# Kernel optimization log

Hardware: AMD Instinct MI355X
Metric: run time of the kernel (lower is better)

## Reference

```python
import jax, jax.numpy as jnp
import numpy as np
import math

V, T, E, H, L = 32000, 1024, 1024, 16, 6
B = 2
D = E // H
F = 4 * E


def setup_inputs() -> dict:
    key = jax.random.key(0)
    ks = jax.random.split(key, 12)
    s = 0.02
    rn = lambda k, shape: jax.random.normal(k, shape, jnp.float32) * s
    return dict(
        idx=jax.random.randint(ks[0], (B, T), 0, V),
        tok_w=rn(ks[1], (V, E)),
        pos_w=rn(ks[2], (T, E)),
        ln1_g=jnp.ones((L, E)), ln1_b=jnp.zeros((L, E)),
        wq=rn(ks[3], (L, E, E)), wk=rn(ks[4], (L, E, E)), wv=rn(ks[5], (L, E, E)),
        wp=rn(ks[6], (L, E, E)), bp=jnp.zeros((L, E)),
        ln2_g=jnp.ones((L, E)), ln2_b=jnp.zeros((L, E)),
        w1=rn(ks[7], (L, E, F)), b1=jnp.zeros((L, F)),
        w2=rn(ks[8], (L, F, E)), b2=jnp.zeros((L, E)),
        lnf_g=jnp.ones((E,)), lnf_b=jnp.zeros((E,)),
        wlm=rn(ks[9], (E, V)), blm=jnp.zeros((V,)),
    )


def _layernorm(x, g, b, eps=1e-5):
    m = jnp.mean(x, axis=-1, keepdims=True)
    v = jnp.var(x, axis=-1, keepdims=True)
    return (x - m) * jax.lax.rsqrt(v + eps) * g + b


def _forward(idx, tok_w, pos_w, ln1_g, ln1_b, wq, wk, wv, wp, bp,
             ln2_g, ln2_b, w1, b1, w2, b2, lnf_g, lnf_b, wlm, blm):
    Bx, Tx = idx.shape
    x = tok_w[idx] + pos_w[jnp.arange(Tx)][None, :, :]  # [B,T,E]
    causal = jnp.tril(jnp.ones((Tx, Tx), dtype=bool))
    scale = 1.0 / math.sqrt(D)
    for l in range(L):
        h = _layernorm(x, ln1_g[l], ln1_b[l])
        q = (h @ wq[l]).reshape(Bx, Tx, H, D).transpose(0, 2, 1, 3)  # [B,H,T,D]
        k = (h @ wk[l]).reshape(Bx, Tx, H, D).transpose(0, 2, 1, 3)
        v = (h @ wv[l]).reshape(Bx, Tx, H, D).transpose(0, 2, 1, 3)
        att = jnp.einsum('bhtd,bhsd->bhts', q, k) * scale  # [B,H,T,T]
        att = jnp.where(causal, att, -jnp.inf)
        att = jax.nn.softmax(att, axis=-1)
        y = jnp.einsum('bhts,bhsd->bhtd', att, v)
        y = y.transpose(0, 2, 1, 3).reshape(Bx, Tx, E)
        x = x + y @ wp[l] + bp[l]
        h2 = _layernorm(x, ln2_g[l], ln2_b[l])
        ff = jax.nn.gelu(h2 @ w1[l] + b1[l], approximate=False) @ w2[l] + b2[l]
        x = x + ff
    x = _layernorm(x, lnf_g, lnf_b)
    return x @ wlm + blm  # logits [B,T,V]


def reference(idx, tok_w, pos_w, ln1_g, ln1_b, wq, wk, wv, wp, bp,
              ln2_g, ln2_b, w1, b1, w2, b2, lnf_g, lnf_b, wlm, blm):
    return _forward(idx, tok_w, pos_w, ln1_g, ln1_b, wq, wk, wv, wp, bp,
                    ln2_g, ln2_b, w1, b1, w2, b2, lnf_g, lnf_b, wlm, blm)
```

## Files before the change

### kernel.cpp

```cpp
#include <hip/hip_runtime.h>

#define T_SEQ   1024
#define E_DIM   1024
#define H_HEADS 16
#define D_HEAD  64
#define L_LAYERS 6
#define B_BATCH 2
#define F_DIM   4096
#define V_VOCAB 32000

typedef float f32x4 __attribute__((ext_vector_type(4)));
typedef short short8 __attribute__((ext_vector_type(8)));

__device__ __forceinline__ unsigned short f2bf(float f) {
  union { float f; unsigned int u; } v; v.f = f;
  unsigned int r = v.u + 0x7fffu + ((v.u >> 16) & 1u);
  return (unsigned short)(r >> 16);
}

#define GLDS16(gp, lp) __builtin_amdgcn_global_load_lds( \
    (const __attribute__((address_space(1))) void*)(gp), \
    (__attribute__((address_space(3))) void*)(lp), 16, 0, 0)

__global__ void embed_kernel(const int* __restrict__ idx, const float* __restrict__ tok,
                             const float* __restrict__ pos, float* __restrict__ x) {
  int i = blockIdx.x * 256 + threadIdx.x;
  int bt = i >> 8;
  int e4 = i & 255;
  int t  = bt & (T_SEQ - 1);
  int tokid = idx[bt];
  f32x4 a = *(const f32x4*)(tok + (size_t)tokid * E_DIM + e4 * 4);
  f32x4 p = *(const f32x4*)(pos + (size_t)t * E_DIM + e4 * 4);
  *(f32x4*)(x + (size_t)bt * E_DIM + e4 * 4) = a + p;
}

__global__ void ln_kernel(const float* __restrict__ x, const float* __restrict__ g,
                          const float* __restrict__ b, unsigned short* __restrict__ out) {
  int row = blockIdx.x;
  int tid = threadIdx.x;
  const float* xr = x + (size_t)row * E_DIM;
  f32x4 v = *(const f32x4*)(xr + tid * 4);
  float s  = v[0] + v[1] + v[2] + v[3];
  float s2 = v[0]*v[0] + v[1]*v[1] + v[2]*v[2] + v[3]*v[3];
  #pragma unroll
  for (int off = 32; off > 0; off >>= 1) {
    s  += __shfl_xor(s,  off);
    s2 += __shfl_xor(s2, off);
  }
  __shared__ float red[2][4];
  int wave = tid >> 6;
  if ((tid & 63) == 0) { red[0][wave] = s; red[1][wave] = s2; }
  __syncthreads();
  s  = red[0][0] + red[0][1] + red[0][2] + red[0][3];
  s2 = red[1][0] + red[1][1] + red[1][2] + red[1][3];
  float mean = s * (1.0f / E_DIM);
  float var  = s2 * (1.0f / E_DIM) - mean * mean;
  float rstd = rsqrtf(var + 1e-5f);
  f32x4 gv = *(const f32x4*)(g + tid * 4);
  f32x4 bv = *(const f32x4*)(b + tid * 4);
  ushort4 o;
  o.x = f2bf((v[0] - mean) * rstd * gv[0] + bv[0]);
  o.y = f2bf((v[1] - mean) * rstd * gv[1] + bv[1]);
  o.z = f2bf((v[2] - mean) * rstd * gv[2] + bv[2]);
  o.w = f2bf((v[3] - mean) * rstd * gv[3] + bv[3]);
  *(ushort4*)(out + (size_t)row * E_DIM + tid * 4) = o;
}

__device__ __forceinline__ void wtrans_body(const float* __restrict__ W,
    unsigned short* __restrict__ Wt, int K, int N, int bx, int by) {
  __shared__ float tile[64][65];
  const int n0 = bx * 64, k0 = by * 64;
  const int tr  = threadIdx.x >> 4;
  const int tc4 = (threadIdx.x & 15) * 4;
  #pragma unroll
  for (int p = 0; p < 4; ++p) {
    f32x4 v = *(const f32x4*)(W + (size_t)(k0 + p * 16 + tr) * N + n0 + tc4);
    tile[p * 16 + tr][tc4 + 0] = v[0];
    tile[p * 16 + tr][tc4 + 1] = v[1];
    tile[p * 16 + tr][tc4 + 2] = v[2];
    tile[p * 16 + tr][tc4 + 3] = v[3];
  }
  __syncthreads();
  #pragma unroll
  for (int p = 0; p < 4; ++p) {
    int n = p * 16 + tr;
    ushort4 o;
    o.x = f2bf(tile[tc4 + 0][n]);
    o.y = f2bf(tile[tc4 + 1][n]);
    o.z = f2bf(tile[tc4 + 2][n]);
    o.w = f2bf(tile[tc4 + 3][n]);
    *(ushort4*)(Wt + (size_t)(n0 + n) * K + k0 + tc4) = o;
  }
}

__global__ __launch_bounds__(256) void wtrans_kernel(const float* __restrict__ W,
    unsigned short* __restrict__ Wt, int K, int N) {
  wtrans_body(W, Wt, K, N, blockIdx.x, blockIdx.y);
}

__global__ __launch_bounds__(256) void wtrans4_kernel(const float* __restrict__ W0,
    const float* __restrict__ W1, const float* __restrict__ W2, const float* __restrict__ W3,
    unsigned short* __restrict__ Wt) {
  const float* W = blockIdx.z == 0 ? W0 : (blockIdx.z == 1 ? W1 : (blockIdx.z == 2 ? W2 : W3));
  wtrans_body(W, Wt + (size_t)blockIdx.z * E_DIM * E_DIM, E_DIM, E_DIM,
              blockIdx.x, blockIdx.y);
}

__global__ __launch_bounds__(256) void wtrans2_kernel(const float* __restrict__ W1,
    const float* __restrict__ W2, unsigned short* __restrict__ Wt1,
    unsigned short* __restrict__ Wt2) {
  const int id = blockIdx.x;
  if (blockIdx.y == 0) wtrans_body(W1, Wt1, E_DIM, F_DIM, id % (F_DIM / 64), id / (F_DIM / 64));
  else                 wtrans_body(W2, Wt2, F_DIM, E_DIM, id % (E_DIM / 64), id / (E_DIM / 64));
}

__global__ __launch_bounds__(512) void attn_mfma_kernel(
    const unsigned short* __restrict__ qk, const unsigned short* __restrict__ vt,
    unsigned short* __restrict__ y) {
  __shared__ __align__(16) char smem[2 * 16384 + 8 * 1280 + 512];
  const int tid  = threadIdx.x;
  const int lane = tid & 63;
  const int wave = tid >> 6;
  const int wl = wave & 3;
  const int g  = wave >> 2;
  const int qx = blockIdx.x;
  const int h  = blockIdx.y & (H_HEADS - 1);
  const int b  = blockIdx.y >> 4;
  const int qt = b ? (15 - qx) : qx;
  const int r0 = qt * 64 + wl * 16;
  const size_t RS = 2 * E_DIM;
  const unsigned short* q  = qk + (size_t)b * T_SEQ * RS + (size_t)h * D_HEAD;
  const unsigned short* k  = q + E_DIM;
  const unsigned short* vb = vt + (size_t)(b * H_HEADS + h) * D_HEAD * T_SEQ;
  const size_t ybase = (size_t)b * T_SEQ * E_DIM + (size_t)h * D_HEAD;
  const int fr = lane & 15, fg = lane >> 4;
  const int srow = lane >> 3;
  const int ssw  = ((lane & 7) * 16) ^ (srow << 4);
  char* pb = smem + 32768 + wave * 1280;
  float* mlb = (float*)(smem + 32768 + 10240);

  short8 aq[2];
  #pragma unroll
  for (int c = 0; c < 2; ++c)
    aq[c] = *(const short8*)(q + (size_t)(r0 + fr) * RS + c * 32 + fg * 8);

  f32x4 oacc[4];
  #pragma unroll
  for (int cg = 0; cg < 4; ++cg) oacc[cg] = (f32x4){0.f, 0.f, 0.f, 0.f};
  float m_ = -1e30f, l_ = 0.0f;

  auto stage = [&](int t) {
    const int j0 = t * 64;
    char* Kd = smem + (t & 1) * 16384;
    GLDS16((const char*)k  + (size_t)(j0 + wave * 8 + srow) * RS * 2 + ssw,
           Kd + wave * 1024);
    GLDS16((const char*)vb + ((size_t)(wave * 8 + srow) * T_SEQ + j0) * 2 + ssw,
           Kd + 8192 + wave * 1024);
  };

  stage(0);
  for (int t = 0; t <= qt; ++t) {
    __builtin_amdgcn_sched_barrier(0);
    __builtin_amdgcn_s_barrier();
    if (t < qt) stage(t + 1);
    __builtin_amdgcn_sched_barrier(0);
    if (t < qt) asm volatile("s_waitcnt vmcnt(2)" ::: "memory");
    else        asm volatile("s_waitcnt vmcnt(0)" ::: "memory");
    __builtin_amdgcn_sched_barrier(0);
    __builtin_amdgcn_s_barrier();
    __builtin_amdgcn_sched_barrier(0);
    const char* Kl = smem + (t & 1) * 16384;
    const char* Vl = Kl + 8192;
    const int j0 = t * 64;
    if (!(t == qt && g == 1 && wl < 2)) {
      f32x4 st[2];
      #pragma unroll
      for (int cc = 0; cc < 2; ++cc) {
        const int kloc = g * 32 + cc * 16 + fr;
        const char* kb = Kl + kloc * 128;
        const int sw = (kloc & 7) << 4;
        short8 ka0 = *(const short8*)(kb + ((fg * 16) ^ sw));
        short8 ka1 = *(const short8*)(kb + ((64 + fg * 16) ^ sw));
        f32x4 z = (f32x4){0.f, 0.f, 0.f, 0.f};
        z = __builtin_amdgcn_mfma_f32_16x16x32_bf16(ka0, aq[0], z, 0, 0, 0);
        z = __builtin_amdgcn_mfma_f32_16x16x32_bf16(ka1, aq[1], z, 0, 0, 0);
        st[cc] = z;
      }
      const int qg = r0 + fr;
      float pv[2][4];
      float mx = -1e30f;
      #pragma unroll
      for (int cc = 0; cc < 2; ++cc)
        #pragma unroll
        for (int r = 0; r < 4; ++r) {
          const int kj = j0 + g * 32 + cc * 16 + fg * 4 + r;
          float val = (kj <= qg) ? st[cc][r] * 0.125f : -1e30f;
          pv[cc][r] = val;
          mx = fmaxf(mx, val);
        }
      mx = fmaxf(mx, __shfl_xor(mx, 16));
      mx = fmaxf(mx, __shfl_xor(mx, 32));
      const float mn = fmaxf(m_, mx);
      const float cfs = __expf(m_ - mn);
      float ls = 0.0f;
      #pragma unroll
      for (int cc = 0; cc < 2; ++cc) {
        ushort4 o;
        float e0 = pv[cc][0] > -1e29f ? __expf(pv[cc][0] - mn) : 0.0f;
        float e1 = pv[cc][1] > -1e29f ? __expf(pv[cc][1] - mn) : 0.0f;
        float e2 = pv[cc][2] > -1e29f ? __expf(pv[cc][2] - mn) : 0.0f;
        float e3 = pv[cc][3] > -1e29f ? __expf(pv[cc][3] - mn) : 0.0f;
        ls += (e0 + e1) + (e2 + e3);
        o.x = f2bf(e0); o.y = f2bf(e1); o.z = f2bf(e2); o.w = f2bf(e3);
        *(ushort4*)(pb + fr * 80 + cc * 32 + fg * 8) = o;
      }
      ls += __shfl_xor(ls, 16);
      ls += __shfl_xor(ls, 32);
      l_ = l_ * cfs + ls;
      m_ = mn;
      float cfO[4];
      #pragma unroll
      for (int r = 0; r < 4; ++r) cfO[r] = __shfl(cfs, (lane & 48) | (fg * 4 + r));
      asm volatile("s_waitcnt lgkmcnt(0)" ::: "memory");
      __builtin_amdgcn_sched_barrier(0);
      short8 pa = *(const short8*)(pb + fr * 80 + fg * 16);
      __builtin_amdgcn_s_setprio(1);
      #pragma unroll
      for (int cg = 0; cg < 4; ++cg) {
        const int d = cg * 16 + fr;
        short8 bv = *(const short8*)(Vl + d * 128 + ((g * 64 + fg * 16) ^ ((d & 7) << 4)));
        #pragma unroll
        for (int r = 0; r < 4; ++r) oacc[cg][r] *= cfO[r];
        oacc[cg] = __builtin_amdgcn_mfma_f32_16x16x32_bf16(pa, bv, oacc[cg], 0, 0, 0);
      }
      __builtin_amdgcn_s_setprio(0);
    }
  }
  __syncthreads();
  float* obuf = (float*)smem;
  if (g == 1) {
    #pragma unroll
    for (int cg = 0; cg < 4; ++cg)
      #pragma unroll
      for (int r = 0; r < 4; ++r)
        obuf[wl * 1024 + (fg * 4 + r) * 64 + cg * 16 + fr] = oacc[cg][r];
    if (fg == 0) { mlb[(wl * 16 + fr) * 2] = m_; mlb[(wl * 16 + fr) * 2 + 1] = l_; }
  }
  __syncthreads();
  if (g == 0) {
    const float m1 = mlb[(wl * 16 + fr) * 2];
    const float l1 = mlb[(wl * 16 + fr) * 2 + 1];
    const float m  = fmaxf(m_, m1);
    const float c0 = __expf(m_ - m), c1 = __expf(m1 - m);
    const float li = 1.0f / (l_ * c0 + l1 * c1);
    float c0O[4], c1O[4], liO[4];
    #pragma unroll
    for (int r = 0; r < 4; ++r) {
      const int src = (lane & 48) | (fg * 4 + r);
      c0O[r] = __shfl(c0, src); c1O[r] = __shfl(c1, src); liO[r] = __shfl(li, src);
    }
    #pragma unroll
    for (int cg = 0; cg < 4; ++cg)
      #pragma unroll
      for (int r = 0; r < 4; ++r) {
        const float o1 = obuf[wl * 1024 + (fg * 4 + r) * 64 + cg * 16 + fr];
        const float val = (oacc[cg][r] * c0O[r] + o1 * c1O[r]) * liO[r];
        y[ybase + (size_t)(r0 + fg * 4 + r) * E_DIM + cg * 16 + fr] = f2bf(val);
      }
  }
}

template<int BM, int BN, bool HAS_BIAS, bool GELU_ACT, bool HAS_RES, int OMODE>
__global__ __launch_bounds__(256) void gemm_bt_kernel(
    const unsigned short* __restrict__ A, const unsigned short* __restrict__ Bt,
    const float* __restrict__ bias, const float* __restrict__ res,
    void* __restrict__ out, unsigned short* __restrict__ vt, int M, int N, int K) {
  constexpr int BK = 64;
  constexpr int MR = BM / 32;
  constexpr int NR = BN / 32;
  constexpr int AI = BM / 32;
  constexpr int BI = BN / 32;
  __shared__ __align__(16) unsigned short As[BM * BK];
  __shared__ __align__(16) unsigned short Bs[BN * BK];
  const int tid  = threadIdx.x;
  const int lane = tid & 63;
  const int wave = tid >> 6;
  const int wr = wave >> 1, wc = wave & 1;

  const int mt = M / BM;
  const int q8 = gridDim.x >> 3;
  const int g  = (blockIdx.x & 7) * q8 + (blockIdx.x >> 3);
  const int m0 = (g % mt) * BM, n0 = (g / mt) * BN;

  const int fr = lane & 15, fg = lane >> 4;
  const int lrow = lane >> 3;
  const int scol = ((lane & 7) * 16) ^ (lrow << 4);
  const size_t K2 = (size_t)K * 2;
  const char* aG = (const char*)A  + (size_t)(m0 + wave * 8 + lrow) * K2 + scol;
  const char* bG = (const char*)Bt + (size_t)(n0 + wave * 8 + lrow) * K2 + scol;

  f32x4 acc[MR][NR];
  #pragma unroll
  for (int mi = 0; mi < MR; ++mi)
    #pragma unroll
    for (int ni = 0; ni < NR; ++ni) acc[mi][ni] = (f32x4){0.f, 0.f, 0.f, 0.f};

  for (int k0 = 0; k0 < K; k0 += BK) {
    __syncthreads();
    #pragma unroll
    for (int i = 0; i < AI; ++i)
      GLDS16(aG + (size_t)i * 32 * K2 + (size_t)k0 * 2, (char*)As + wave * 1024 + i * 4096);
    #pragma unroll
    for (int i = 0; i < BI; ++i)
      GLDS16(bG + (size_t)i * 32 * K2 + (size_t)k0 * 2, (char*)Bs + wave * 1024 + i * 4096);
    __syncthreads();

    short8 af[MR][2], bf[NR][2];
    #pragma unroll
    for (int mi = 0; mi < MR; ++mi) {
      const int row = wr * (BM / 2) + mi * 16 + fr;
      #pragma unroll
      for (int kh = 0; kh < 2; ++kh)
        af[mi][kh] = *(const short8*)((const char*)As + row * 128 +
                       ((kh * 64 + fg * 16) ^ ((row & 7) << 4)));
    }
    #pragma unroll
    for (int ni = 0; ni < NR; ++ni) {
      const int row = wc * (BN / 2) + ni * 16 + fr;
      #pragma unroll
      for (int kh = 0; kh < 2; ++kh)
        bf[ni][kh] = *(const short8*)((const char*)Bs + row * 128 +
                       ((kh * 64 + fg * 16) ^ ((row & 7) << 4)));
    }
    #pragma unroll
    for (int mi = 0; mi < MR; ++mi)
      #pragma unroll
      for (int ni = 0; ni < NR; ++ni) {
        acc[mi][ni] = __builtin_amdgcn_mfma_f32_16x16x32_bf16(af[mi][0], bf[ni][0], acc[mi][ni], 0, 0, 0);
        acc[mi][ni] = __builtin_amdgcn_mfma_f32_16x16x32_bf16(af[mi][1], bf[ni][1], acc[mi][ni], 0, 0, 0);
      }
  }

  #pragma unroll
  for (int mi = 0; mi < MR; ++mi) {
    #pragma unroll
    for (int ni = 0; ni < NR; ++ni) {
      const int col = n0 + wc * (BN / 2) + ni * 16 + fr;
      float bv = HAS_BIAS ? bias[col] : 0.0f;
      float vals[4];
      const int rbase = m0 + wr * (BM / 2) + mi * 16 + fg * 4;
      #pragma unroll
      for (int r = 0; r < 4; ++r) {
        float val = acc[mi][ni][r] + bv;
        if (GELU_ACT) val = 0.5f * val * (1.0f + erff(val * 0.70710678118f));
        if (HAS_RES)  val += res[(size_t)(rbase + r) * N + col];
        vals[r] = val;
      }
      if (OMODE == 0) {
        #pragma unroll
        for (int r = 0; r < 4; ++r)
          ((float*)out)[(size_t)(rbase + r) * N + col] = vals[r];
      } else if (OMODE == 1) {
        #pragma unroll
        for (int r = 0; r < 4; ++r)
          ((unsigned short*)out)[(size_t)(rbase + r) * N + col] = f2bf(vals[r]);
      } else {
        if (col < 2 * E_DIM) {
          #pragma unroll
          for (int r = 0; r < 4; ++r)
            ((unsigned short*)out)[(size_t)(rbase + r) * 2 * E_DIM + col] = f2bf(vals[r]);
        } else {
          const int c2 = col - 2 * E_DIM;
          const int hh = c2 >> 6, d = c2 & 63;
          const int bb = rbase >> 10, t0 = rbase & (T_SEQ - 1);
          ushort4 o;
          o.x = f2bf(vals[0]); o.y = f2bf(vals[1]);
          o.z = f2bf(vals[2]); o.w = f2bf(vals[3]);
          *(ushort4*)(vt + ((size_t)(bb * H_HEADS + hh) * D_HEAD + d) * T_SEQ + t0) = o;
        }
      }
    }
  }
}

__global__ __launch_bounds__(512, 1) void gemm8p_kernel(
    const unsigned short* __restrict__ A, const unsigned short* __restrict__ Bt,
    const float* __restrict__ bias, float* __restrict__ out, int M, int N, int K) {
  __shared__ __align__(16) char lds[131072];
  const int tid  = threadIdx.x;
  const int lane = tid & 63;
  const int wv   = tid >> 6;
  const int wm = wv >> 2, wn = wv & 3;

  const int mt = M >> 8;
  const int q8 = gridDim.x >> 3;
  const int g  = (blockIdx.x & 7) * q8 + (blockIdx.x >> 3);
  const int m0 = (g % mt) * 256, n0 = (g / mt) * 256;

  const int fr = lane & 15, fg = lane >> 4;
  const size_t K2 = (size_t)K * 2;
  const int nIter = K >> 7;

  const int csw0 = (fg * 16) ^ ((fr & 7) << 4);
  const int csw1 = (64 + fg * 16) ^ ((fr & 7) << 4);

  const int sc = (lane * 16) & 127;
  const size_t laneoff = (size_t)(lane >> 3) * K2 + (size_t)(sc ^ ((lane >> 3) << 4));
  const char* Asrc = (const char*)(A + (size_t)m0 * K) + (size_t)(wv * 8) * K2 + laneoff;
  const char* Bsrc = (const char*)(Bt + (size_t)n0 * K) + laneoff;

  f32x4 acc[8][4];
  #pragma unroll
  for (int i = 0; i < 8; ++i)
    #pragma unroll
    for (int j = 0; j < 4; ++j) acc[i][j] = (f32x4){0.f, 0.f, 0.f, 0.f};

  auto stageA = [&](int b, int q, int kt) {
    GLDS16(Asrc + (size_t)(q * 64) * K2 + (size_t)kt * 128,
           lds + b * 65536 + q * 8192 + wv * 1024);
  };
  auto stageB = [&](int b, int j, int o, int kt) {
    const int gw = j * 64 + wv * 8;
    const int rw = ((gw >> 5) << 6) + (gw & 31) + o * 32;
    GLDS16(Bsrc + (size_t)rw * K2 + (size_t)kt * 128,
           lds + b * 65536 + 32768 + rw * 128);
  };

  stageA(0, 0, 0); stageA(0, 2, 0);
  stageB(0, 0, 0, 0); stageB(0, 1, 0, 0);
  stageA(0, 1, 0); stageA(0, 3, 0);
  stageB(0, 0, 1, 0); stageB(0, 1, 1, 0);
  stageA(1, 0, 1); stageA(1, 2, 1);
  stageB(1, 0, 0, 1); stageB(1, 1, 0, 1);
  __builtin_amdgcn_sched_barrier(0);
  asm volatile("s_waitcnt vmcnt(4)" ::: "memory");
  __builtin_amdgcn_s_barrier();

  for (int i = 0; i < nIter; ++i) {
    const bool last = (i == nIter - 1);
    #pragma unroll
    for (int p = 0; p < 8; ++p) {
      const int b  = p >> 2;
      const int mh = (p & 3) >> 1;
      const int nh = p & 1;
      const char* Ab = lds + b * 65536;
      const char* Bb = Ab + 32768;
      __builtin_amdgcn_sched_barrier(0);
      short8 fa[4][2], fb[2][2];
      #pragma unroll
      for (int j = 0; j < 4; ++j) {
        const int row = wm * 128 + mh * 64 + j * 16 + fr;
        fa[j][0] = *(const short8*)(Ab + row * 128 + csw0);
        fa[j][1] = *(const short8*)(Ab + row * 128 + csw1);
      }
      #pragma unroll
      for (int n = 0; n < 2; ++n) {
        const int row = wn * 64 + nh * 32 + n * 16 + fr;
        fb[n][0] = *(const short8*)(Bb + row * 128 + csw0);
        fb[n][1] = *(const short8*)(Bb + row * 128 + csw1);
      }
      if (p == 0) { stageA(1, 1, 2 * i + 1); stageA(1, 3, 2 * i + 1); }
      if (p == 1) { stageB(1, 0, 1, 2 * i + 1); stageB(1, 1, 1, 2 * i + 1); }
      if (!last) {
        if (p == 2) { stageA(0, 0, 2 * i + 2); stageA(0, 2, 2 * i + 2); }
        if (p == 3) { stageB(0, 0, 0, 2 * i + 2); stageB(0, 1, 0, 2 * i + 2); }
        if (p == 4) { stageA(0, 1, 2 * i + 2); stageA(0, 3, 2 * i + 2); }
        if (p == 5) { stageB(0, 0, 1, 2 * i + 2); stageB(0, 1, 1, 2 * i + 2); }
        if (p == 6) { stageA(1, 0, 2 * i + 3); stageA(1, 2, 2 * i + 3); }
        if (p == 7) { stageB(1, 0, 0, 2 * i + 3); stageB(1, 1, 0, 2 * i + 3); }
      }
      __builtin_amdgcn_sched_barrier(0);
      __builtin_amdgcn_s_barrier();
      __builtin_amdgcn_sched_barrier(0);
      __builtin_amdgcn_s_setprio(1);
      #pragma unroll
      for (int j = 0; j < 4; ++j)
        #pragma unroll
        for (int n = 0; n < 2; ++n) {
          acc[mh * 4 + j][nh * 2 + n] = __builtin_amdgcn_mfma_f32_16x16x32_bf16(
              fa[j][0], fb[n][0], acc[mh * 4 + j][nh * 2 + n], 0, 0, 0);
          acc[mh * 4 + j][nh * 2 + n] = __builtin_amdgcn_mfma_f32_16x16x32_bf16(
              fa[j][1], fb[n][1], acc[mh * 4 + j][nh * 2 + n], 0, 0, 0);
        }
      __builtin_amdgcn_s_setprio(0);
      __builtin_amdgcn_sched_barrier(0);
      if (p == 3) {
        if (!last) asm volatile("s_waitcnt vmcnt(4)" ::: "memory");
        else       asm volatile("s_waitcnt vmcnt(0)" ::: "memory");
      }
      if (p == 7 && !last)
        asm volatile("s_waitcnt vmcnt(4)" ::: "memory");
      __builtin_amdgcn_s_barrier();
    }
  }

  #pragma unroll
  for (int mi = 0; mi < 8; ++mi) {
    #pragma unroll
    for (int ni = 0; ni < 4; ++ni) {
      const int col = n0 + wn * 64 + ni * 16 + fr;
      const float bv = bias[col];
      #pragma unroll
      for (int r = 0; r < 4; ++r) {
        const int row = m0 + wm * 128 + mi * 16 + fg * 4 + r;
        out[(size_t)row * N + col] = acc[mi][ni][r] + bv;
      }
    }
  }
}

extern "C" void kernel_launch(void* const* d_in, const int* in_sizes, int n_in,
                              void* d_out, int out_size, void* d_ws, size_t ws_size,
                              hipStream_t stream) {
  const int*   idx   = (const int*)  d_in[0];
  const float* tok_w = (const float*)d_in[1];
  const float* pos_w = (const float*)d_in[2];
  const float* ln1_g = (const float*)d_in[3];
  const float* ln1_b = (const float*)d_in[4];
  const float* wq    = (const float*)d_in[5];
  const float* wk    = (const float*)d_in[6];
  const float* wv    = (const float*)d_in[7];
  const float* wp    = (const float*)d_in[8];
  const float* bp    = (const float*)d_in[9];
  const float* ln2_g = (const float*)d_in[10];
  const float* ln2_b = (const float*)d_in[11];
  const float* w1    = (const float*)d_in[12];
  const float* b1    = (const float*)d_in[13];
  const float* w2    = (const float*)d_in[14];
  const float* b2    = (const float*)d_in[15];
  const float* lnf_g = (const float*)d_in[16];
  const float* lnf_b = (const float*)d_in[17];
  const float* wlm   = (const float*)d_in[18];
  const float* blm   = (const float*)d_in[19];

  const int M = B_BATCH * T_SEQ;
  const size_t EE = (size_t)E_DIM * E_DIM;
  const size_t EF = (size_t)E_DIM * F_DIM;
  char* p = (char*)d_ws;
  float* x            = (float*)p;          p += (size_t)M * E_DIM * 4;
  unsigned short* hb  = (unsigned short*)p; p += (size_t)M * E_DIM * 2;
  unsigned short* qkb = (unsigned short*)p; p += (size_t)M * 2 * E_DIM * 2;
  unsigned short* vtb = (unsigned short*)p; p += (size_t)M * E_DIM * 2;
  unsigned short* yb  = (unsigned short*)p; p += (size_t)M * E_DIM * 2;
  unsigned short* tb  = (unsigned short*)p; p += (size_t)M * F_DIM * 2;
  unsigned short* wtb = (unsigned short*)p; p += (size_t)V_VOCAB * E_DIM * 2;

  embed_kernel<<<M * E_DIM / 4 / 256, 256, 0, stream>>>(idx, tok_w, pos_w, x);

  for (int l = 0; l < L_LAYERS; ++l) {
    ln_kernel<<<M, 256, 0, stream>>>(x, ln1_g + (size_t)l * E_DIM, ln1_b + (size_t)l * E_DIM, hb);
    wtrans4_kernel<<<dim3(E_DIM / 64, E_DIM / 64, 4), 256, 0, stream>>>(
        wq + l * EE, wk + l * EE, wv + l * EE, wp + l * EE, wtb);
    gemm_bt_kernel<128, 128, false, false, false, 2>
        <<<(M / 128) * (3 * E_DIM / 128), 256, 0, stream>>>(
        hb, wtb, nullptr, nullptr, qkb, vtb, M, 3 * E_DIM, E_DIM);
    attn_mfma_kernel<<<dim3(16, B_BATCH * H_HEADS), 512, 0, stream>>>(qkb, vtb, yb);
    gemm_bt_kernel<64, 128, true, false, true, 0>
        <<<(M / 64) * (E_DIM / 128), 256, 0, stream>>>(
        yb, wtb + 3 * EE, bp + (size_t)l * E_DIM, x, x, nullptr, M, E_DIM, E_DIM);
    ln_kernel<<<M, 256, 0, stream>>>(x, ln2_g + (size_t)l * E_DIM, ln2_b + (size_t)l * E_DIM, hb);
    wtrans2_kernel<<<dim3(1024, 2), 256, 0, stream>>>(
        w1 + l * EF, w2 + l * EF, wtb, wtb + EF);
    gemm_bt_kernel<128, 128, true, true, false, 1>
        <<<(M / 128) * (F_DIM / 128), 256, 0, stream>>>(
        hb, wtb, b1 + (size_t)l * F_DIM, nullptr, tb, nullptr, M, F_DIM, E_DIM);
    gemm_bt_kernel<64, 128, true, false, true, 0>
        <<<(M / 64) * (E_DIM / 128), 256, 0, stream>>>(
        tb, wtb + EF, b2 + (size_t)l * E_DIM, x, x, nullptr, M, E_DIM, F_DIM);
  }
  ln_kernel<<<M, 256, 0, stream>>>(x, lnf_g, lnf_b, hb);
  wtrans_kernel<<<dim3(V_VOCAB / 64, E_DIM / 64), 256, 0, stream>>>(wlm, wtb, E_DIM, V_VOCAB);
  gemm8p_kernel<<<(M / 256) * (V_VOCAB / 256), 512, 0, stream>>>(
      hb, wtb, blm, (float*)d_out, M, V_VOCAB, E_DIM);
}
```

Baseline: 1.325 ms.

## Use 8-wave 128x256 pipelined MFMA GEMM for QKV and FFN1, merge weight transposes

Adds a new 512-thread GEMM kernel with 128x256 tiles, double-buffered direct-to-LDS loads, fine-grained phase scheduling and wave priority. It replaces the 128x128 GEMM for the QKV projection and the first FFN matmul. It also fuses the two per-layer weight-transpose launches into one 6-matrix kernel issued at the start of each layer, which needs a larger workspace layout. The bigger tiles increase data reuse, but the fewer blocks may under-fill the GPU, and the workspace offsets have changed.

```diff
diff --git a/kernel.cpp b/kernel.cpp
--- a/kernel.cpp
+++ b/kernel.cpp
@@ -98,20 +98,24 @@
   wtrans_body(W, Wt, K, N, blockIdx.x, blockIdx.y);
 }
 
-__global__ __launch_bounds__(256) void wtrans4_kernel(const float* __restrict__ W0,
-    const float* __restrict__ W1, const float* __restrict__ W2, const float* __restrict__ W3,
-    unsigned short* __restrict__ Wt) {
-  const float* W = blockIdx.z == 0 ? W0 : (blockIdx.z == 1 ? W1 : (blockIdx.z == 2 ? W2 : W3));
-  wtrans_body(W, Wt + (size_t)blockIdx.z * E_DIM * E_DIM, E_DIM, E_DIM,
-              blockIdx.x, blockIdx.y);
-}
-
-__global__ __launch_bounds__(256) void wtrans2_kernel(const float* __restrict__ W1,
-    const float* __restrict__ W2, unsigned short* __restrict__ Wt1,
-    unsigned short* __restrict__ Wt2) {
+__global__ __launch_bounds__(256) void wtrans6_kernel(const float* __restrict__ wq,
+    const float* __restrict__ wk, const float* __restrict__ wv, const float* __restrict__ wp,
+    const float* __restrict__ w1, const float* __restrict__ w2,
+    unsigned short* __restrict__ wtb) {
+  const size_t EE = (size_t)E_DIM * E_DIM;
+  const size_t EF = (size_t)E_DIM * F_DIM;
   const int id = blockIdx.x;
-  if (blockIdx.y == 0) wtrans_body(W1, Wt1, E_DIM, F_DIM, id % (F_DIM / 64), id / (F_DIM / 64));
-  else                 wtrans_body(W2, Wt2, F_DIM, E_DIM, id % (E_DIM / 64), id / (E_DIM / 64));
+  if (id < 1024) {
+    const int z = id >> 8, r = id & 255;
+    const float* W = z == 0 ? wq : (z == 1 ? wk : (z == 2 ? wv : wp));
+    wtrans_body(W, wtb + z * EE, E_DIM, E_DIM, r & 15, r >> 4);
+  } else if (id < 2048) {
+    const int r = id - 1024;
+    wtrans_body(w1, wtb + 4 * EE, E_DIM, F_DIM, r & 63, r >> 6);
+  } else {
+    const int r = id - 2048;
+    wtrans_body(w2, wtb + 4 * EE + EF, F_DIM, E_DIM, r & 15, r >> 4);
+  }
 }
 
 __global__ __launch_bounds__(512) void attn_mfma_kernel(
@@ -360,7 +364,140 @@
         #pragma unroll
         for (int r = 0; r < 4; ++r)
           ((float*)out)[(size_t)(rbase + r) * N + col] = vals[r];
-      } else if (OMODE == 1) {
+      } else {
+        #pragma unroll
+        for (int r = 0; r < 4; ++r)
+          ((unsigned short*)out)[(size_t)(rbase + r) * N + col] = f2bf(vals[r]);
+      }
+    }
+  }
+}
+
+template<int OMODE, bool HAS_BIAS, bool GELU_ACT>
+__global__ __launch_bounds__(512, 1) void gemm8p2_kernel(
+    const unsigned short* __restrict__ A, const unsigned short* __restrict__ Bt,
+    const float* __restrict__ bias, void* __restrict__ out,
+    unsigned short* __restrict__ vt, int M, int N, int K) {
+  __shared__ __align__(16) char lds[98304];
+  const int tid  = threadIdx.x;
+  const int lane = tid & 63;
+  const int wv   = tid >> 6;
+  const int wm = wv >> 2, wn = wv & 3;
+
+  const int mt = M >> 7;
+  const int q8 = gridDim.x >> 3;
+  const int g  = (blockIdx.x & 7) * q8 + (blockIdx.x >> 3);
+  const int m0 = (g % mt) * 128, n0 = (g / mt) * 256;
+
+  const int fr = lane & 15, fg = lane >> 4;
+  const size_t K2 = (size_t)K * 2;
+  const int nIter = K >> 7;
+
+  const int csw0 = (fg * 16) ^ ((fr & 7) << 4);
+  const int csw1 = (64 + fg * 16) ^ ((fr & 7) << 4);
+
+  const int sc = (lane * 16) & 127;
+  const size_t laneoff = (size_t)(lane >> 3) * K2 + (size_t)(sc ^ ((lane >> 3) << 4));
+  const char* Asrc = (const char*)(A + (size_t)m0 * K) + laneoff;
+  const char* Bsrc = (const char*)(Bt + (size_t)n0 * K) + laneoff;
+  const int arow_wv = (wv >> 2) * 64 + (wv & 3) * 8;
+  const int brow_wv = (wv >> 2) * 64 + (wv & 3) * 8;
+
+  f32x4 acc[4][4];
+  #pragma unroll
+  for (int i = 0; i < 4; ++i)
+    #pragma unroll
+    for (int j = 0; j < 4; ++j) acc[i][j] = (f32x4){0.f, 0.f, 0.f, 0.f};
+
+  auto stageA = [&](int b, int c, int kt) {
+    GLDS16(Asrc + (size_t)(arow_wv + c * 32) * K2 + (size_t)kt * 128,
+           lds + b * 49152 + c * 8192 + wv * 1024);
+  };
+  auto stageB = [&](int b, int j, int kt) {
+    GLDS16(Bsrc + (size_t)((j & 1) * 128 + (j >> 1) * 32 + brow_wv) * K2 + (size_t)kt * 128,
+           lds + b * 49152 + 16384 + j * 8192 + wv * 1024);
+  };
+
+  stageA(0, 0, 0); stageA(0, 1, 0);
+  stageB(0, 0, 0); stageB(0, 1, 0); stageB(0, 2, 0); stageB(0, 3, 0);
+  stageA(1, 0, 1); stageB(1, 0, 1); stageB(1, 1, 1);
+  __builtin_amdgcn_sched_barrier(0);
+  asm volatile("s_waitcnt vmcnt(3)" ::: "memory");
+  __builtin_amdgcn_s_barrier();
+
+  for (int i = 0; i < nIter; ++i) {
+    const bool last = (i == nIter - 1);
+    #pragma unroll
+    for (int p = 0; p < 8; ++p) {
+      const int b  = p >> 2;
+      const int mh = (p >> 1) & 1;
+      const int nh = p & 1;
+      const char* Ab = lds + b * 49152;
+      const char* Bb = Ab + 16384;
+      __builtin_amdgcn_sched_barrier(0);
+      short8 fa[2][2], fb[2][2];
+      #pragma unroll
+      for (int j = 0; j < 2; ++j) {
+        const int row = mh * 64 + wm * 32 + j * 16 + fr;
+        fa[j][0] = *(const short8*)(Ab + row * 128 + csw0);
+        fa[j][1] = *(const short8*)(Ab + row * 128 + csw1);
+      }
+      #pragma unroll
+      for (int n = 0; n < 2; ++n) {
+        const int row = nh * 128 + (wn >> 1) * 64 + (wn & 1) * 32 + n * 16 + fr;
+        fb[n][0] = *(const short8*)(Bb + row * 128 + csw0);
+        fb[n][1] = *(const short8*)(Bb + row * 128 + csw1);
+      }
+      if (p == 0) stageA(1, 1, 2 * i + 1);
+      if (p == 1) { stageB(1, 2, 2 * i + 1); stageB(1, 3, 2 * i + 1); }
+      if (!last) {
+        if (p == 2) stageA(0, 0, 2 * i + 2);
+        if (p == 3) { stageB(0, 0, 2 * i + 2); stageB(0, 1, 2 * i + 2); }
+        if (p == 4) stageA(0, 1, 2 * i + 2);
+        if (p == 5) { stageB(0, 2, 2 * i + 2); stageB(0, 3, 2 * i + 2); }
+        if (p == 6) stageA(1, 0, 2 * i + 3);
+        if (p == 7) { stageB(1, 0, 2 * i + 3); stageB(1, 1, 2 * i + 3); }
+      }
+      __builtin_amdgcn_sched_barrier(0);
+      __builtin_amdgcn_s_barrier();
+      __builtin_amdgcn_sched_barrier(0);
+      __builtin_amdgcn_s_setprio(1);
+      #pragma unroll
+      for (int j = 0; j < 2; ++j)
+        #pragma unroll
+        for (int n = 0; n < 2; ++n) {
+          acc[mh * 2 + j][nh * 2 + n] = __builtin_amdgcn_mfma_f32_16x16x32_bf16(
+              fa[j][0], fb[n][0], acc[mh * 2 + j][nh * 2 + n], 0, 0, 0);
+          acc[mh * 2 + j][nh * 2 + n] = __builtin_amdgcn_mfma_f32_16x16x32_bf16(
+              fa[j][1], fb[n][1], acc[mh * 2 + j][nh * 2 + n], 0, 0, 0);
+        }
+      __builtin_amdgcn_s_setprio(0);
+      __builtin_amdgcn_sched_barrier(0);
+      if (p == 3) {
+        if (!last) asm volatile("s_waitcnt vmcnt(3)" ::: "memory");
+        else       asm volatile("s_waitcnt vmcnt(0)" ::: "memory");
+      }
+      if (p == 7 && !last)
+        asm volatile("s_waitcnt vmcnt(3)" ::: "memory");
+      __builtin_amdgcn_s_barrier();
+    }
+  }
+
+  #pragma unroll
+  for (int mi = 0; mi < 4; ++mi) {
+    #pragma unroll
+    for (int ni = 0; ni < 4; ++ni) {
+      const int col = n0 + wn * 64 + ni * 16 + fr;
+      float bv = HAS_BIAS ? bias[col] : 0.0f;
+      const int rbase = m0 + wm * 64 + mi * 16 + fg * 4;
+      float vals[4];
+      #pragma unroll
+      for (int r = 0; r < 4; ++r) {
+        float val = acc[mi][ni][r] + bv;
+        if (GELU_ACT) val = 0.5f * val * (1.0f + erff(val * 0.70710678118f));
+        vals[r] = val;
+      }
+      if (OMODE == 1) {
         #pragma unroll
         for (int r = 0; r < 4; ++r)
           ((unsigned short*)out)[(size_t)(rbase + r) * N + col] = f2bf(vals[r]);
@@ -548,25 +685,24 @@
   embed_kernel<<<M * E_DIM / 4 / 256, 256, 0, stream>>>(idx, tok_w, pos_w, x);
 
   for (int l = 0; l < L_LAYERS; ++l) {
+    wtrans6_kernel<<<3072, 256, 0, stream>>>(
+        wq + l * EE, wk + l * EE, wv + l * EE, wp + l * EE,
+        w1 + l * EF, w2 + l * EF, wtb);
     ln_kernel<<<M, 256, 0, stream>>>(x, ln1_g + (size_t)l * E_DIM, ln1_b + (size_t)l * E_DIM, hb);
-    wtrans4_kernel<<<dim3(E_DIM / 64, E_DIM / 64, 4), 256, 0, stream>>>(
-        wq + l * EE, wk + l * EE, wv + l * EE, wp + l * EE, wtb);
-    gemm_bt_kernel<128, 128, false, false, false, 2>
-        <<<(M / 128) * (3 * E_DIM / 128), 256, 0, stream>>>(
-        hb, wtb, nullptr, nullptr, qkb, vtb, M, 3 * E_DIM, E_DIM);
+    gemm8p2_kernel<2, false, false>
+        <<<(M / 128) * (3 * E_DIM / 256), 512, 0, stream>>>(
+        hb, wtb, nullptr, qkb, vtb, M, 3 * E_DIM, E_DIM);
     attn_mfma_kernel<<<dim3(16, B_BATCH * H_HEADS), 512, 0, stream>>>(qkb, vtb, yb);
     gemm_bt_kernel<64, 128, true, false, true, 0>
         <<<(M / 64) * (E_DIM / 128), 256, 0, stream>>>(
         yb, wtb + 3 * EE, bp + (size_t)l * E_DIM, x, x, nullptr, M, E_DIM, E_DIM);
     ln_kernel<<<M, 256, 0, stream>>>(x, ln2_g + (size_t)l * E_DIM, ln2_b + (size_t)l * E_DIM, hb);
-    wtrans2_kernel<<<dim3(1024, 2), 256, 0, stream>>>(
-        w1 + l * EF, w2 + l * EF, wtb, wtb + EF);
-    gemm_bt_kernel<128, 128, true, true, false, 1>
-        <<<(M / 128) * (F_DIM / 128), 256, 0, stream>>>(
-        hb, wtb, b1 + (size_t)l * F_DIM, nullptr, tb, nullptr, M, F_DIM, E_DIM);
+    gemm8p2_kernel<1, true, true>
+        <<<(M / 128) * (F_DIM / 256), 512, 0, stream>>>(
+        hb, wtb + 4 * EE, b1 + (size_t)l * F_DIM, tb, nullptr, M, F_DIM, E_DIM);
     gemm_bt_kernel<64, 128, true, false, true, 0>
         <<<(M / 64) * (E_DIM / 128), 256, 0, stream>>>(
-        tb, wtb + EF, b2 + (size_t)l * E_DIM, x, x, nullptr, M, E_DIM, F_DIM);
+        tb, wtb + 4 * EE + EF, b2 + (size_t)l * E_DIM, x, x, nullptr, M, E_DIM, F_DIM);
   }
   ln_kernel<<<M, 256, 0, stream>>>(x, lnf_g, lnf_b, hb);
   wtrans_kernel<<<dim3(V_VOCAB / 64, E_DIM / 64), 256, 0, stream>>>(wlm, wtb, E_DIM, V_VOCAB);
```

Measured after the change: 1.297 ms. 1.02x faster.
